# Kernel tuning notes

Measured on AMD Instinct MI355X. Metric: run time of the kernel, lower is better.

## Reference

```python
import jax, jax.numpy as jnp
import numpy as np
from jax import lax

N, C, H, W = 16, 1, 512, 512
MAX_ITERS = H + W  # upper bound on flood-fill propagation distance


def _dilate4(r):
    # 3x3 cross (4-connectivity) grayscale dilation, r: (N,H,W)
    rp = jnp.pad(r, ((0, 0), (1, 1), (1, 1)))
    up = rp[:, :-2, 1:-1]
    dn = rp[:, 2:, 1:-1]
    lf = rp[:, 1:-1, :-2]
    rt = rp[:, 1:-1, 2:]
    return jnp.maximum(jnp.maximum(jnp.maximum(up, dn), jnp.maximum(lf, rt)), r)


def _reconstruct_dilation(marker, mask):
    # skimage.morphology.reconstruction(seed, mask, method='dilation'):
    # iterate rec = min(dilate(rec), mask) until convergence.
    def cond(state):
        _, changed, i = state
        return jnp.logical_and(changed, i < MAX_ITERS)

    def body(state):
        r, _, i = state
        nr = jnp.minimum(_dilate4(r), mask)
        return nr, jnp.any(nr != r), i + 1

    rec, _, _ = lax.while_loop(cond, body, (marker, jnp.array(True), jnp.array(0)))
    return rec


def _adaptive_binarize(prob, marker_factor, mask_factor):
    # prob: (N,1,H,W); mirrors torch .detach() -> threshold -> reconstruction
    img = lax.stop_gradient(prob[:, 0])  # (N,H,W)
    nzm = img > 0
    cnt = jnp.sum(nzm, axis=(1, 2))                      # (N,)
    safe = jnp.maximum(cnt, 1).astype(img.dtype)
    mean = jnp.sum(jnp.where(nzm, img, 0.0), axis=(1, 2)) / safe
    var = jnp.sum(jnp.where(nzm, (img - mean[:, None, None]) ** 2, 0.0), axis=(1, 2)) / safe
    std = jnp.sqrt(var)

    def threshold(factor):
        T = (mean + factor * std)[:, None, None]
        b = img > T
        empty = jnp.sum(b, axis=(1, 2)) == 0
        T2 = (mean + (factor / 2.0) * std)[:, None, None]
        b2 = img > T2
        return jnp.where(empty[:, None, None], b2, b)

    marker = threshold(marker_factor).astype(jnp.float32)
    maskb = threshold(mask_factor).astype(jnp.float32)
    rec = _reconstruct_dilation(marker, maskb)
    out = (rec > 0.5).astype(jnp.float32)
    out = jnp.where((cnt == 0)[:, None, None], 0.0, out)  # no nonzero pixels -> zeros
    return out[:, None]  # (N,1,H,W)


def setup_inputs() -> dict:
    key = jax.random.key(0)
    k1, k2 = jax.random.split(key)
    thick_logit = jax.random.normal(k1, (N, C, H, W), dtype=jnp.float32)
    thin_logit = jax.random.normal(k2, (N, C, H, W), dtype=jnp.float32)
    return {"thick_logit": thick_logit, "thin_logit": thin_logit}


def reference(thick_logit, thin_logit):
    thick_prob = jax.nn.sigmoid(thick_logit)
    thin_prob = jax.nn.sigmoid(thin_logit)
    thick_bin = _adaptive_binarize(thick_prob, 2.0, 0.5)
    thin_bin = _adaptive_binarize(thin_prob, 4.0, 0.5)
    fused_bin = jnp.clip(thick_bin + thin_bin, 0.0, 1.0)
    return thick_logit, thin_logit, fused_bin
```

## Files before the change

kernel.cpp:

```cpp
#include <hip/hip_runtime.h>
#include <cstdint>
#include <cstddef>

#define HW 512
#define NPIX (HW * HW)
#define NIMG 16
#define NII 32
#define CHUNKS 64
#define CHUNK_PIX 4096
#define IN_ELEMS (NIMG * NPIX)
#define WPI 4096

typedef unsigned long long u64;

#define WS_PARTA 0u
#define WS_CUT   65536u
#define WS_ZM    65792u
#define WS_MSEL  98304u
#define WS_KSEL  (WS_MSEL + 1048576u)
#define WS_ROUT  (WS_KSEL + 1048576u)

__device__ __forceinline__ float sigmoid_f32(float x) {
    return (float)(1.0 / (1.0 + exp(-(double)x)));
}

__device__ __forceinline__ float sigmoid_fast(float xf) {
    double x = (double)xf;
    double y = x * -1.4426950408889634074;
    if (y > 1000.0)  return 0.0f;
    if (y < -1000.0) return 1.0f;
    double n = __builtin_rint(y);
    double t = (y - n) * 0.69314718055994530942;
    double p = 2.5052108385441718775e-8;
    p = __builtin_fma(p, t, 2.7557319223985890653e-7);
    p = __builtin_fma(p, t, 2.7557319223985892511e-6);
    p = __builtin_fma(p, t, 2.4801587301587301566e-5);
    p = __builtin_fma(p, t, 1.9841269841269841253e-4);
    p = __builtin_fma(p, t, 1.3888888888888889419e-3);
    p = __builtin_fma(p, t, 8.3333333333333332177e-3);
    p = __builtin_fma(p, t, 4.1666666666666664354e-2);
    p = __builtin_fma(p, t, 1.6666666666666665741e-1);
    p = __builtin_fma(p, t, 5.0e-1);
    p = __builtin_fma(p, t, 1.0);
    p = __builtin_fma(p, t, 1.0);
    long long bits = ((long long)n + 1023ll) << 52;
    double e = p * __longlong_as_double(bits);
    return (float)(1.0 / (1.0 + e));
}

__global__ void k1_copy_stats(const float* __restrict__ A, const float* __restrict__ B,
                              float* __restrict__ out, double* __restrict__ partA) {
    int b = blockIdx.x;
    int ii = b >> 6, chunk = b & 63;
    int j = ii >> 4, n = ii & 15;
    const float* src = (j == 0 ? A : B) + (size_t)n * NPIX + (size_t)chunk * CHUNK_PIX;
    float* dst = out + (size_t)j * IN_ELEMS + (size_t)n * NPIX + (size_t)chunk * CHUNK_PIX;

    double s = 0.0, sq = 0.0, cc = 0.0;
    float mx = -__builtin_inff();
#pragma unroll
    for (int p = 0; p < 4; ++p) {
        float4 v = *(const float4*)(src + p * 1024 + threadIdx.x * 4);
        *(float4*)(dst + p * 1024 + threadIdx.x * 4) = v;
        float xs[4] = {v.x, v.y, v.z, v.w};
#pragma unroll
        for (int q = 0; q < 4; ++q) {
            float img = sigmoid_fast(xs[q]);
            mx = fmaxf(mx, xs[q]);
            if (img > 0.0f) { double d = (double)img; s += d; sq += d * d; cc += 1.0; }
        }
    }
    __shared__ double sm[256], sv[256], sc[256];
    __shared__ float smx[256];
    sm[threadIdx.x] = s; sv[threadIdx.x] = sq; sc[threadIdx.x] = cc; smx[threadIdx.x] = mx;
    __syncthreads();
    for (int off = 128; off > 0; off >>= 1) {
        if (threadIdx.x < off) {
            sm[threadIdx.x] += sm[threadIdx.x + off];
            sv[threadIdx.x] += sv[threadIdx.x + off];
            sc[threadIdx.x] += sc[threadIdx.x + off];
            smx[threadIdx.x] = fmaxf(smx[threadIdx.x], smx[threadIdx.x + off]);
        }
        __syncthreads();
    }
    if (threadIdx.x == 0) {
        double* p = partA + (size_t)(ii * 64 + chunk) * 4;
        p[0] = sm[0]; p[1] = sv[0]; p[2] = sc[0]; p[3] = (double)smx[0];
    }
}

__device__ __forceinline__ float key_to_f32(unsigned k) {
    unsigned b = (k & 0x80000000u) ? (k ^ 0x80000000u) : ~k;
    return __uint_as_float(b);
}
__device__ float find_cut(double T) {
    if (!(1.0 > T)) return __uint_as_float(0x7F800000u);
    unsigned lo = 0x007FFFFFu;
    unsigned hi = 0xFF800000u;
    while (lo < hi) {
        unsigned mid = lo + ((hi - lo) >> 1);
        float x = key_to_f32(mid);
        float s32 = sigmoid_f32(x);
        if ((double)s32 > T) hi = mid; else lo = mid + 1;
    }
    return key_to_f32(lo);
}

__global__ void kS_cut(const double* __restrict__ partA,
                       float* __restrict__ cut2, u64* __restrict__ zm) {
    int ii = blockIdx.x, t = threadIdx.x;
    const double* p = partA + (size_t)(ii * 64 + t) * 4;
    double s = p[0], sq = p[1], c = p[2], mx = p[3];
    for (int off = 32; off > 0; off >>= 1) {
        s  += __shfl_down(s,  (unsigned)off, 64);
        sq += __shfl_down(sq, (unsigned)off, 64);
        c  += __shfl_down(c,  (unsigned)off, 64);
        mx  = fmax(mx, __shfl_down(mx, (unsigned)off, 64));
    }
    s = __shfl(s, 0, 64); sq = __shfl(sq, 0, 64);
    c = __shfl(c, 0, 64); mx = __shfl(mx, 0, 64);
    double mean = 0.0, sd = 0.0;
    if (c > 0.0) {
        mean = s / c;
        double var = sq / c - mean * mean;
        if (var < 0.0) var = 0.0;
        sd = sqrt(var);
    }
    double fac = (ii < 16) ? 2.0 : 4.0;
    __shared__ float cs[4];
    if (t < 4) {
        double T = (t == 0) ? mean + fac * sd
                 : (t == 1) ? mean + 0.5 * fac * sd
                 : (t == 2) ? mean + 0.5 * sd
                 :            mean + 0.25 * sd;
        cs[t] = find_cut(T);
    }
    __syncthreads();
    if (t == 0) {
        float mxf = (float)mx;
        cut2[ii * 2 + 0] = (mxf >= cs[0]) ? cs[0] : cs[1];
        cut2[ii * 2 + 1] = (mxf >= cs[2]) ? cs[2] : cs[3];
        zm[ii] = (c > 0.0) ? ~0ull : 0ull;
    }
}

__global__ void k2_bits(const float* __restrict__ A, const float* __restrict__ B,
                        const float* __restrict__ cut2,
                        u64* __restrict__ msel, u64* __restrict__ ksel) {
    int b = blockIdx.x, ii = b >> 6, chunk = b & 63;
    int j = ii >> 4, n = ii & 15;
    const float* src = (j == 0 ? A : B) + (size_t)n * NPIX;
    float cM = cut2[ii * 2 + 0];
    float cK = cut2[ii * 2 + 1];
    int t = threadIdx.x, lane = t & 63, w = t >> 6;
#pragma unroll 4
    for (int i = 0; i < 16; ++i) {
        float x = src[chunk * CHUNK_PIX + i * 256 + t];
        u64 bM = __ballot(x >= cM);
        u64 bK = __ballot(x >= cK);
        if (lane == 0) {
            size_t g = (size_t)ii * WPI + (size_t)chunk * 64 + i * 4 + w;
            msel[g] = bM; ksel[g] = bK;
        }
    }
}

__device__ __forceinline__ void hfill8(u64* x, const u64* k) {
    u64 c = 0;
#pragma unroll
    for (int w = 0; w < 8; ++w) {
        u64 a = k[w], g = x[w];
        u64 t1 = a + g;  u64 c1 = (u64)(t1 < a);
        u64 t2 = t1 + c; u64 c2 = (u64)(t2 < t1);
        c = c1 | c2;
        x[w] = (~t2 | g) & a;
    }
    c = 0;
#pragma unroll
    for (int w = 7; w >= 0; --w) {
        u64 a = __brevll(k[w]), g = __brevll(x[w]);
        u64 t1 = a + g;  u64 c1 = (u64)(t1 < a);
        u64 t2 = t1 + c; u64 c2 = (u64)(t2 < t1);
        c = c1 | c2;
        x[w] = __brevll((~t2 | g) & a);
    }
}

__global__ __launch_bounds__(512) void k3_flood(const u64* __restrict__ msel,
                                                const u64* __restrict__ ksel,
                                                u64* __restrict__ rout) {
    int ii = blockIdx.x, t = threadIdx.x;
    __shared__ u64 R[8 * HW];
    const u64* M = msel + (size_t)ii * WPI;
    const u64* K = ksel + (size_t)ii * WPI;

    u64 r[8], k[8];
#pragma unroll
    for (int w = 0; w < 8; ++w) {
        k[w] = K[(size_t)t * 8 + w];
        r[w] = M[(size_t)t * 8 + w] & k[w];
    }
    hfill8(r, k);
#pragma unroll
    for (int w = 0; w < 8; ++w) R[w * HW + t] = r[w];
    __syncthreads();

    for (int it = 0; it < 1024; ++it) {
        u64 up[8], dn[8];
#pragma unroll
        for (int w = 0; w < 8; ++w) {
            up[w] = (t > 0)      ? R[w * HW + (t - 1)] : 0ull;
            dn[w] = (t < HW - 1) ? R[w * HW + (t + 1)] : 0ull;
        }
        __syncthreads();
        u64 diff = 0;
#pragma unroll
        for (int w = 0; w < 8; ++w) {
            u64 g = (up[w] | dn[w]) & k[w] & ~r[w];
            r[w] |= g; diff |= g;
        }
        if (diff) {
            hfill8(r, k);
#pragma unroll
            for (int w = 0; w < 8; ++w) R[w * HW + t] = r[w];
        }
        if (!__syncthreads_or(diff != 0ull ? 1 : 0)) break;
    }

#pragma unroll
    for (int w = 0; w < 8; ++w)
        rout[(size_t)ii * WPI + (size_t)w * HW + t] = r[w];
}

__global__ void k4_fuse(const u64* __restrict__ rout,
                        const u64* __restrict__ zm,
                        float* __restrict__ out) {
    size_t gid = (size_t)blockIdx.x * blockDim.x + threadIdx.x;
    size_t p = gid * 4;
    int n = (int)(p >> 18);
    int e = (int)(p & (NPIX - 1));
    size_t gw = (size_t)(((e >> 6) & 7) * HW + (e >> 9));
    u64 w = (rout[(size_t)n * WPI + gw] & zm[n])
          | (rout[(size_t)(16 + n) * WPI + gw] & zm[16 + n]);
    int sh = e & 63;
    float4 v;
    v.x = ((w >> sh) & 1ull)       ? 1.0f : 0.0f;
    v.y = ((w >> (sh + 1)) & 1ull) ? 1.0f : 0.0f;
    v.z = ((w >> (sh + 2)) & 1ull) ? 1.0f : 0.0f;
    v.w = ((w >> (sh + 3)) & 1ull) ? 1.0f : 0.0f;
    *(float4*)(out + 2 * (size_t)IN_ELEMS + p) = v;
}

extern "C" void kernel_launch(void* const* d_in, const int* in_sizes, int n_in,
                              void* d_out, int out_size, void* d_ws, size_t ws_size,
                              hipStream_t stream) {
    const float* A = (const float*)d_in[0];
    const float* B = (const float*)d_in[1];
    float* out = (float*)d_out;
    char* ws = (char*)d_ws;

    double* partA = (double*)(ws + WS_PARTA);
    float*  cut2  = (float*)(ws + WS_CUT);
    u64*    zm    = (u64*)(ws + WS_ZM);
    u64*    msel  = (u64*)(ws + WS_MSEL);
    u64*    ksel  = (u64*)(ws + WS_KSEL);
    u64*    rout  = (u64*)(ws + WS_ROUT);

    k1_copy_stats<<<NII * CHUNKS, 256, 0, stream>>>(A, B, out, partA);
    kS_cut<<<NII, 64, 0, stream>>>(partA, cut2, zm);
    k2_bits<<<NII * CHUNKS, 256, 0, stream>>>(A, B, cut2, msel, ksel);
    k3_flood<<<NII, 512, 0, stream>>>(msel, ksel, rout);
    k4_fuse<<<4096, 256, 0, stream>>>(rout, zm, out);
}
```

Baseline: 145.7 us.

## Flood fill by alternating full-row fills on transposed bitplanes; fold cut kernel into bits

The flood-fill loop now transposes the 512x512 bit image in shared memory each phase, using 64x64 bit transposes done with wave shuffles. It then runs the carry-propagating full-segment fill along rows and along columns in turn. This replaces the one-row-per-iteration vertical propagation, so far fewer iterations should be needed on winding regions. The threshold/cut computation kernel is also merged into the bitmask kernel: every block recomputes the reductions and the binary search, which removes one launch but repeats that work across 2048 blocks.

```diff
diff --git a/kernel.cpp b/kernel.cpp
--- a/kernel.cpp
+++ b/kernel.cpp
@@ -14,8 +14,7 @@
 typedef unsigned long long u64;
 
 #define WS_PARTA 0u
-#define WS_CUT   65536u
-#define WS_ZM    65792u
+#define WS_ZM    65536u
 #define WS_MSEL  98304u
 #define WS_KSEL  (WS_MSEL + 1048576u)
 #define WS_ROUT  (WS_KSEL + 1048576u)
@@ -106,29 +105,44 @@
     return key_to_f32(lo);
 }
 
-__global__ void kS_cut(const double* __restrict__ partA,
-                       float* __restrict__ cut2, u64* __restrict__ zm) {
-    int ii = blockIdx.x, t = threadIdx.x;
-    const double* p = partA + (size_t)(ii * 64 + t) * 4;
-    double s = p[0], sq = p[1], c = p[2], mx = p[3];
-    for (int off = 32; off > 0; off >>= 1) {
-        s  += __shfl_down(s,  (unsigned)off, 64);
-        sq += __shfl_down(sq, (unsigned)off, 64);
-        c  += __shfl_down(c,  (unsigned)off, 64);
-        mx  = fmax(mx, __shfl_down(mx, (unsigned)off, 64));
-    }
-    s = __shfl(s, 0, 64); sq = __shfl(sq, 0, 64);
-    c = __shfl(c, 0, 64); mx = __shfl(mx, 0, 64);
-    double mean = 0.0, sd = 0.0;
-    if (c > 0.0) {
-        mean = s / c;
-        double var = sq / c - mean * mean;
-        if (var < 0.0) var = 0.0;
-        sd = sqrt(var);
-    }
-    double fac = (ii < 16) ? 2.0 : 4.0;
+__global__ void k2_bits(const float* __restrict__ A, const float* __restrict__ B,
+                        const double* __restrict__ partA,
+                        u64* __restrict__ msel, u64* __restrict__ ksel,
+                        u64* __restrict__ zm) {
+    int b = blockIdx.x, ii = b >> 6, chunk = b & 63;
+    int j = ii >> 4, n = ii & 15;
+    const float* src = (j == 0 ? A : B) + (size_t)n * NPIX;
+    int t = threadIdx.x, lane = t & 63, w = t >> 6;
+
+    __shared__ double shst[4];
     __shared__ float cs[4];
+    __shared__ float cut2[2];
+
+    if (t < 64) {
+        const double* p = partA + (size_t)(ii * 64 + t) * 4;
+        double s = p[0], sq = p[1], c = p[2], mx = p[3];
+#pragma unroll
+        for (int off = 32; off > 0; off >>= 1) {
+            s  += __shfl_down(s,  (unsigned)off, 64);
+            sq += __shfl_down(sq, (unsigned)off, 64);
+            c  += __shfl_down(c,  (unsigned)off, 64);
+            mx  = fmax(mx, __shfl_down(mx, (unsigned)off, 64));
+        }
+        if (t == 0) {
+            double mean = 0.0, sd = 0.0;
+            if (c > 0.0) {
+                mean = s / c;
+                double var = sq / c - mean * mean;
+                if (var < 0.0) var = 0.0;
+                sd = sqrt(var);
+            }
+            shst[0] = mean; shst[1] = sd; shst[2] = c; shst[3] = mx;
+        }
+    }
+    __syncthreads();
     if (t < 4) {
+        double mean = shst[0], sd = shst[1];
+        double fac = (ii < 16) ? 2.0 : 4.0;
         double T = (t == 0) ? mean + fac * sd
                  : (t == 1) ? mean + 0.5 * fac * sd
                  : (t == 2) ? mean + 0.5 * sd
@@ -137,22 +151,14 @@
     }
     __syncthreads();
     if (t == 0) {
-        float mxf = (float)mx;
-        cut2[ii * 2 + 0] = (mxf >= cs[0]) ? cs[0] : cs[1];
-        cut2[ii * 2 + 1] = (mxf >= cs[2]) ? cs[2] : cs[3];
-        zm[ii] = (c > 0.0) ? ~0ull : 0ull;
-    }
-}
-
-__global__ void k2_bits(const float* __restrict__ A, const float* __restrict__ B,
-                        const float* __restrict__ cut2,
-                        u64* __restrict__ msel, u64* __restrict__ ksel) {
-    int b = blockIdx.x, ii = b >> 6, chunk = b & 63;
-    int j = ii >> 4, n = ii & 15;
-    const float* src = (j == 0 ? A : B) + (size_t)n * NPIX;
-    float cM = cut2[ii * 2 + 0];
-    float cK = cut2[ii * 2 + 1];
-    int t = threadIdx.x, lane = t & 63, w = t >> 6;
+        float mxf = (float)shst[3];
+        cut2[0] = (mxf >= cs[0]) ? cs[0] : cs[1];
+        cut2[1] = (mxf >= cs[2]) ? cs[2] : cs[3];
+        if (chunk == 0) zm[ii] = (shst[2] > 0.0) ? ~0ull : 0ull;
+    }
+    __syncthreads();
+    float cM = cut2[0], cK = cut2[1];
+
 #pragma unroll 4
     for (int i = 0; i < 16; ++i) {
         float x = src[chunk * CHUNK_PIX + i * 256 + t];
@@ -186,50 +192,104 @@
     }
 }
 
+__device__ __forceinline__ u64 tr64(u64 x, int lane) {
+    const u64 MS[6] = { 0x00000000FFFFFFFFull, 0x0000FFFF0000FFFFull,
+                        0x00FF00FF00FF00FFull, 0x0F0F0F0F0F0F0F0Full,
+                        0x3333333333333333ull, 0x5555555555555555ull };
+#pragma unroll
+    for (int i = 0; i < 6; ++i) {
+        int s = 32 >> i;
+        u64 m = MS[i];
+        u64 y = __shfl_xor(x, s, 64);
+        u64 a = (x & m) | ((y & m) << s);
+        u64 bq = (x & ~m) | ((y & ~m) >> s);
+        x = (lane & s) ? bq : a;
+    }
+    return x;
+}
+
+__device__ void transpose512(u64* BUF, int t) {
+    int lane = t & 63, wv = t >> 6;
+    int c = 0;
+#pragma unroll
+    for (int I = 0; I < 8; ++I) {
+#pragma unroll
+        for (int J = I; J < 8; ++J) {
+            if ((c & 7) == wv) {
+                if (I == J) {
+                    u64 v = BUF[J * 512 + 64 * I + lane];
+                    v = tr64(v, lane);
+                    BUF[J * 512 + 64 * I + lane] = v;
+                } else {
+                    u64 a = BUF[J * 512 + 64 * I + lane];
+                    u64 b = BUF[I * 512 + 64 * J + lane];
+                    a = tr64(a, lane);
+                    b = tr64(b, lane);
+                    BUF[J * 512 + 64 * I + lane] = b;
+                    BUF[I * 512 + 64 * J + lane] = a;
+                }
+            }
+            ++c;
+        }
+    }
+}
+
 __global__ __launch_bounds__(512) void k3_flood(const u64* __restrict__ msel,
                                                 const u64* __restrict__ ksel,
                                                 u64* __restrict__ rout) {
     int ii = blockIdx.x, t = threadIdx.x;
-    __shared__ u64 R[8 * HW];
+    __shared__ u64 BUF[WPI];
     const u64* M = msel + (size_t)ii * WPI;
     const u64* K = ksel + (size_t)ii * WPI;
 
-    u64 r[8], k[8];
+    u64 kr[8], kc[8], r[8];
 #pragma unroll
     for (int w = 0; w < 8; ++w) {
-        k[w] = K[(size_t)t * 8 + w];
-        r[w] = M[(size_t)t * 8 + w] & k[w];
-    }
-    hfill8(r, k);
-#pragma unroll
-    for (int w = 0; w < 8; ++w) R[w * HW + t] = r[w];
-    __syncthreads();
-
-    for (int it = 0; it < 1024; ++it) {
-        u64 up[8], dn[8];
+        kr[w] = K[(size_t)t * 8 + w];
+        BUF[w * 512 + t] = kr[w];
+    }
+    __syncthreads();
+    transpose512(BUF, t);
+    __syncthreads();
+#pragma unroll
+    for (int w = 0; w < 8; ++w) kc[w] = BUF[w * 512 + t];
+    __syncthreads();
+
+#pragma unroll
+    for (int w = 0; w < 8; ++w) r[w] = M[(size_t)t * 8 + w] & kr[w];
+    hfill8(r, kr);
+#pragma unroll
+    for (int w = 0; w < 8; ++w) BUF[w * 512 + t] = r[w];
+
+    int orient = 0;
+    for (int ph = 0; ph < 1200; ++ph) {
+        __syncthreads();
+        transpose512(BUF, t);
+        orient ^= 1;
+        __syncthreads();
+        u64 rr[8], d = 0;
+#pragma unroll
+        for (int w = 0; w < 8; ++w) rr[w] = BUF[w * 512 + t];
+        u64 old[8];
+#pragma unroll
+        for (int w = 0; w < 8; ++w) old[w] = rr[w];
+        hfill8(rr, orient ? kc : kr);
 #pragma unroll
         for (int w = 0; w < 8; ++w) {
-            up[w] = (t > 0)      ? R[w * HW + (t - 1)] : 0ull;
-            dn[w] = (t < HW - 1) ? R[w * HW + (t + 1)] : 0ull;
-        }
-        __syncthreads();
-        u64 diff = 0;
-#pragma unroll
-        for (int w = 0; w < 8; ++w) {
-            u64 g = (up[w] | dn[w]) & k[w] & ~r[w];
-            r[w] |= g; diff |= g;
-        }
-        if (diff) {
-            hfill8(r, k);
-#pragma unroll
-            for (int w = 0; w < 8; ++w) R[w * HW + t] = r[w];
-        }
-        if (!__syncthreads_or(diff != 0ull ? 1 : 0)) break;
-    }
-
+            d |= rr[w] ^ old[w];
+            BUF[w * 512 + t] = rr[w];
+        }
+        if (!__syncthreads_or(d != 0ull ? 1 : 0)) break;
+    }
+
+    if (orient == 1) {
+        __syncthreads();
+        transpose512(BUF, t);
+        __syncthreads();
+    }
 #pragma unroll
     for (int w = 0; w < 8; ++w)
-        rout[(size_t)ii * WPI + (size_t)w * HW + t] = r[w];
+        rout[(size_t)ii * WPI + (size_t)w * 512 + t] = BUF[w * 512 + t];
 }
 
 __global__ void k4_fuse(const u64* __restrict__ rout,
@@ -260,15 +320,13 @@
     char* ws = (char*)d_ws;
 
     double* partA = (double*)(ws + WS_PARTA);
-    float*  cut2  = (float*)(ws + WS_CUT);
     u64*    zm    = (u64*)(ws + WS_ZM);
     u64*    msel  = (u64*)(ws + WS_MSEL);
     u64*    ksel  = (u64*)(ws + WS_KSEL);
     u64*    rout  = (u64*)(ws + WS_ROUT);
 
     k1_copy_stats<<<NII * CHUNKS, 256, 0, stream>>>(A, B, out, partA);
-    kS_cut<<<NII, 64, 0, stream>>>(partA, cut2, zm);
-    k2_bits<<<NII * CHUNKS, 256, 0, stream>>>(A, B, cut2, msel, ksel);
+    k2_bits<<<NII * CHUNKS, 256, 0, stream>>>(A, B, partA, msel, ksel, zm);
     k3_flood<<<NII, 512, 0, stream>>>(msel, ksel, rout);
     k4_fuse<<<4096, 256, 0, stream>>>(rout, zm, out);
 }
```

New measurement: 207.5 us. +42.5%, slower.

## Fuse cut computation into bit kernel and batch flood sweeps per barrier

Applied to the files above, without the earlier changes.

Removes the separate stats/cut kernel by having every k2_bits block redo the partial reduction and threshold binary search, which saves a launch but repeats that work per chunk. The flood-fill loop now does four unsynchronized propagation sweeps between block-wide OR barriers, cutting barrier count. Those sweeps read neighbours' shared rows while they are being written; this relies on the fill being monotone. sigmoid_fast's division is replaced with rcp plus Newton refinement.

```diff
diff --git a/kernel.cpp b/kernel.cpp
--- a/kernel.cpp
+++ b/kernel.cpp
@@ -14,8 +14,7 @@
 typedef unsigned long long u64;
 
 #define WS_PARTA 0u
-#define WS_CUT   65536u
-#define WS_ZM    65792u
+#define WS_ZM    65536u
 #define WS_MSEL  98304u
 #define WS_KSEL  (WS_MSEL + 1048576u)
 #define WS_ROUT  (WS_KSEL + 1048576u)
@@ -45,7 +44,13 @@
     p = __builtin_fma(p, t, 1.0);
     long long bits = ((long long)n + 1023ll) << 52;
     double e = p * __longlong_as_double(bits);
-    return (float)(1.0 / (1.0 + e));
+    double d = 1.0 + e;
+    if (y > 100.0 || y < -100.0)
+        return (float)(1.0 / d);
+    double r = (double)__builtin_amdgcn_rcpf((float)d);
+    r = r * (2.0 - d * r);
+    r = r * (2.0 - d * r);
+    return (float)r;
 }
 
 __global__ void k1_copy_stats(const float* __restrict__ A, const float* __restrict__ B,
@@ -106,29 +111,44 @@
     return key_to_f32(lo);
 }
 
-__global__ void kS_cut(const double* __restrict__ partA,
-                       float* __restrict__ cut2, u64* __restrict__ zm) {
-    int ii = blockIdx.x, t = threadIdx.x;
-    const double* p = partA + (size_t)(ii * 64 + t) * 4;
-    double s = p[0], sq = p[1], c = p[2], mx = p[3];
-    for (int off = 32; off > 0; off >>= 1) {
-        s  += __shfl_down(s,  (unsigned)off, 64);
-        sq += __shfl_down(sq, (unsigned)off, 64);
-        c  += __shfl_down(c,  (unsigned)off, 64);
-        mx  = fmax(mx, __shfl_down(mx, (unsigned)off, 64));
-    }
-    s = __shfl(s, 0, 64); sq = __shfl(sq, 0, 64);
-    c = __shfl(c, 0, 64); mx = __shfl(mx, 0, 64);
-    double mean = 0.0, sd = 0.0;
-    if (c > 0.0) {
-        mean = s / c;
-        double var = sq / c - mean * mean;
-        if (var < 0.0) var = 0.0;
-        sd = sqrt(var);
-    }
-    double fac = (ii < 16) ? 2.0 : 4.0;
+__global__ void k2_bits(const float* __restrict__ A, const float* __restrict__ B,
+                        const double* __restrict__ partA,
+                        u64* __restrict__ msel, u64* __restrict__ ksel,
+                        u64* __restrict__ zm) {
+    int b = blockIdx.x, ii = b >> 6, chunk = b & 63;
+    int j = ii >> 4, n = ii & 15;
+    const float* src = (j == 0 ? A : B) + (size_t)n * NPIX;
+    int t = threadIdx.x, lane = t & 63, w = t >> 6;
+
+    __shared__ double shst[4];
     __shared__ float cs[4];
+    __shared__ float cut2[2];
+
+    if (t < 64) {
+        const double* p = partA + (size_t)(ii * 64 + t) * 4;
+        double s = p[0], sq = p[1], c = p[2], mx = p[3];
+#pragma unroll
+        for (int off = 32; off > 0; off >>= 1) {
+            s  += __shfl_down(s,  (unsigned)off, 64);
+            sq += __shfl_down(sq, (unsigned)off, 64);
+            c  += __shfl_down(c,  (unsigned)off, 64);
+            mx  = fmax(mx, __shfl_down(mx, (unsigned)off, 64));
+        }
+        if (t == 0) {
+            double mean = 0.0, sd = 0.0;
+            if (c > 0.0) {
+                mean = s / c;
+                double var = sq / c - mean * mean;
+                if (var < 0.0) var = 0.0;
+                sd = sqrt(var);
+            }
+            shst[0] = mean; shst[1] = sd; shst[2] = c; shst[3] = mx;
+        }
+    }
+    __syncthreads();
     if (t < 4) {
+        double mean = shst[0], sd = shst[1];
+        double fac = (ii < 16) ? 2.0 : 4.0;
         double T = (t == 0) ? mean + fac * sd
                  : (t == 1) ? mean + 0.5 * fac * sd
                  : (t == 2) ? mean + 0.5 * sd
@@ -137,22 +157,14 @@
     }
     __syncthreads();
     if (t == 0) {
-        float mxf = (float)mx;
-        cut2[ii * 2 + 0] = (mxf >= cs[0]) ? cs[0] : cs[1];
-        cut2[ii * 2 + 1] = (mxf >= cs[2]) ? cs[2] : cs[3];
-        zm[ii] = (c > 0.0) ? ~0ull : 0ull;
-    }
-}
-
-__global__ void k2_bits(const float* __restrict__ A, const float* __restrict__ B,
-                        const float* __restrict__ cut2,
-                        u64* __restrict__ msel, u64* __restrict__ ksel) {
-    int b = blockIdx.x, ii = b >> 6, chunk = b & 63;
-    int j = ii >> 4, n = ii & 15;
-    const float* src = (j == 0 ? A : B) + (size_t)n * NPIX;
-    float cM = cut2[ii * 2 + 0];
-    float cK = cut2[ii * 2 + 1];
-    int t = threadIdx.x, lane = t & 63, w = t >> 6;
+        float mxf = (float)shst[3];
+        cut2[0] = (mxf >= cs[0]) ? cs[0] : cs[1];
+        cut2[1] = (mxf >= cs[2]) ? cs[2] : cs[3];
+        if (chunk == 0) zm[ii] = (shst[2] > 0.0) ? ~0ull : 0ull;
+    }
+    __syncthreads();
+    float cM = cut2[0], cK = cut2[1];
+
 #pragma unroll 4
     for (int i = 0; i < 16; ++i) {
         float x = src[chunk * CHUNK_PIX + i * 256 + t];
@@ -205,26 +217,27 @@
     for (int w = 0; w < 8; ++w) R[w * HW + t] = r[w];
     __syncthreads();
 
-    for (int it = 0; it < 1024; ++it) {
-        u64 up[8], dn[8];
-#pragma unroll
-        for (int w = 0; w < 8; ++w) {
-            up[w] = (t > 0)      ? R[w * HW + (t - 1)] : 0ull;
-            dn[w] = (t < HW - 1) ? R[w * HW + (t + 1)] : 0ull;
-        }
-        __syncthreads();
-        u64 diff = 0;
-#pragma unroll
-        for (int w = 0; w < 8; ++w) {
-            u64 g = (up[w] | dn[w]) & k[w] & ~r[w];
-            r[w] |= g; diff |= g;
-        }
-        if (diff) {
-            hfill8(r, k);
-#pragma unroll
-            for (int w = 0; w < 8; ++w) R[w * HW + t] = r[w];
-        }
-        if (!__syncthreads_or(diff != 0ull ? 1 : 0)) break;
+    for (int round = 0; round < 256; ++round) {
+        u64 gained = 0;
+#pragma unroll 1
+        for (int sweep = 0; sweep < 4; ++sweep) {
+            u64 diff = 0;
+#pragma unroll
+            for (int w = 0; w < 8; ++w) {
+                u64 nb = (t > 0      ? R[w * HW + (t - 1)] : 0ull)
+                       | (t < HW - 1 ? R[w * HW + (t + 1)] : 0ull);
+                u64 g = nb & k[w] & ~r[w];
+                r[w] |= g; diff |= g;
+            }
+            if (diff) {
+                hfill8(r, k);
+#pragma unroll
+                for (int w = 0; w < 8; ++w) R[w * HW + t] = r[w];
+                gained |= diff;
+            }
+            asm volatile("" ::: "memory");
+        }
+        if (!__syncthreads_or(gained != 0ull ? 1 : 0)) break;
     }
 
 #pragma unroll
@@ -260,15 +273,13 @@
     char* ws = (char*)d_ws;
 
     double* partA = (double*)(ws + WS_PARTA);
-    float*  cut2  = (float*)(ws + WS_CUT);
     u64*    zm    = (u64*)(ws + WS_ZM);
     u64*    msel  = (u64*)(ws + WS_MSEL);
     u64*    ksel  = (u64*)(ws + WS_KSEL);
     u64*    rout  = (u64*)(ws + WS_ROUT);
 
     k1_copy_stats<<<NII * CHUNKS, 256, 0, stream>>>(A, B, out, partA);
-    kS_cut<<<NII, 64, 0, stream>>>(partA, cut2, zm);
-    k2_bits<<<NII * CHUNKS, 256, 0, stream>>>(A, B, cut2, msel, ksel);
+    k2_bits<<<NII * CHUNKS, 256, 0, stream>>>(A, B, partA, msel, ksel, zm);
     k3_flood<<<NII, 512, 0, stream>>>(msel, ksel, rout);
     k4_fuse<<<4096, 256, 0, stream>>>(rout, zm, out);
 }
```

Measured after the change: 141.5 us. -2.9%, faster.
